# Kernel optimization log

Hardware: AMD Instinct MI355X
Metric: run time of the kernel (lower is better)

Reference implementation:

```python
import jax, jax.numpy as jnp
import numpy as np

N_E = 1024
E_DIM = 64
BETA = 0.25


def setup_inputs() -> dict:
    key = jax.random.key(0)
    k1, k2 = jax.random.split(key)
    z = jax.random.normal(k1, (32, 32, 32, E_DIM), dtype=jnp.float32)
    # torch init: uniform(-1/n_e, 1/n_e)
    codebook = jax.random.uniform(k2, (N_E, E_DIM), dtype=jnp.float32,
                                  minval=-1.0 / N_E, maxval=1.0 / N_E)
    return {"z": z, "codebook": codebook}


def reference(z, codebook):
    z_flat = z.reshape(-1, E_DIM)  # [N, e_dim]
    # squared euclidean distances: ||z||^2 + ||e||^2 - 2 z e^T
    d = (jnp.sum(z_flat ** 2, axis=1, keepdims=True)
         + jnp.sum(codebook ** 2, axis=1)
         - 2.0 * jnp.matmul(z_flat, codebook.T))  # [N, n_e]
    idx = jnp.argmin(d, axis=1)  # [N]
    z_q = codebook[idx].reshape(z.shape)
    sg = jax.lax.stop_gradient
    loss = jnp.mean((sg(z_q) - z) ** 2) + BETA * jnp.mean((z_q - sg(z)) ** 2)
    z_q_st = z + sg(z_q - z)  # straight-through estimator
    return z_q_st, idx, loss
```

## Files before the change

kernel.cpp:

```cpp
#include <hip/hip_runtime.h>

#define NROWS 32768
#define NE    1024
#define ED    64
#define CHUNK 256
#define NCH   (NE / CHUNK)
#define RPW   8

typedef float4 f4;

__global__ void vq_prep(const float* __restrict__ cb, float* __restrict__ ssq)
{
    int j = blockIdx.x * blockDim.x + threadIdx.x;
    const f4* crow = (const f4*)(cb + (size_t)j * ED);
    float v[ED];
#pragma unroll
    for (int i = 0; i < 16; ++i) {
        f4 t = crow[i];
        v[4*i+0] = t.x; v[4*i+1] = t.y; v[4*i+2] = t.z; v[4*i+3] = t.w;
    }
    {
#pragma clang fp contract(off)
        float r0 = v[0]*v[0], r1 = v[1]*v[1], r2 = v[2]*v[2], r3 = v[3]*v[3];
        float r4 = v[4]*v[4], r5 = v[5]*v[5], r6 = v[6]*v[6], r7 = v[7]*v[7];
#pragma unroll
        for (int i = 8; i < ED; i += 8) {
            r0 += v[i+0]*v[i+0]; r1 += v[i+1]*v[i+1];
            r2 += v[i+2]*v[i+2]; r3 += v[i+3]*v[i+3];
            r4 += v[i+4]*v[i+4]; r5 += v[i+5]*v[i+5];
            r6 += v[i+6]*v[i+6]; r7 += v[i+7]*v[i+7];
        }
        ssq[j] = ((r0+r1)+(r2+r3)) + ((r4+r5)+(r6+r7));
    }
}

__global__ __launch_bounds__(256, 2)
void vq_main(const float* __restrict__ z, const float* __restrict__ cb,
             const float* __restrict__ ssq, float* __restrict__ out,
             float* __restrict__ partials)
{
    __shared__ __align__(16) float et[ED * CHUNK];
    __shared__ __align__(16) float sqsh[NE];
    __shared__ int   idxsh[32];
    __shared__ float wsum[4];

    const int tid  = threadIdx.x;
    const int lane = tid & 63;
    const int w    = tid >> 6;
    const int w_u  = __builtin_amdgcn_readfirstlane(w);
    const int rowbase = blockIdx.x * 32;

    ((f4*)sqsh)[tid] = ((const f4*)ssq)[tid];

    float cn[RPW];
    {
        const int rl = lane >> 3;
        const int jj = lane & 7;
        const float* zr = z + (size_t)(rowbase + w_u * RPW + rl) * ED;
        float a;
        {
#pragma clang fp contract(off)
            a = 0.f;
#pragma unroll
            for (int i = 0; i < 8; ++i) { float v = zr[8*i + jj]; a += v*v; }
        }
        a += __shfl_xor(a, 1);
        a += __shfl_xor(a, 2);
        a += __shfl_xor(a, 4);
#pragma unroll
        for (int r = 0; r < RPW; ++r) cn[r] = __shfl(a, r * 8);
    }

    float bestv[RPW];
    int   besti[RPW];
#pragma unroll
    for (int r = 0; r < RPW; ++r) { bestv[r] = INFINITY; besti[r] = 0; }

    const f4* et4 = (const f4*)et;
    const float* zw = z + (size_t)(rowbase + w_u * RPW) * ED;

    for (int ch = 0; ch < NCH; ++ch) {
        __syncthreads();
        {
            const f4* crow = (const f4*)(cb + (size_t)(ch * CHUNK + tid) * ED);
#pragma unroll
            for (int i = 0; i < 16; ++i) {
                f4 t = crow[i];
                et[(4*i+0) * CHUNK + tid] = t.x;
                et[(4*i+1) * CHUNK + tid] = t.y;
                et[(4*i+2) * CHUNK + tid] = t.z;
                et[(4*i+3) * CHUNK + tid] = t.w;
            }
        }
        __syncthreads();

        f4 sv = ((const f4*)sqsh)[ch * 64 + lane];
        float svq[4] = {sv.x, sv.y, sv.z, sv.w};

        float acc[RPW][4];
#pragma unroll
        for (int r = 0; r < RPW; ++r)
            acc[r][0] = acc[r][1] = acc[r][2] = acc[r][3] = 0.f;

#pragma unroll 2
        for (int k4 = 0; k4 < 16; ++k4) {
            f4 e0 = et4[(4*k4+0) * 64 + lane];
            f4 e1 = et4[(4*k4+1) * 64 + lane];
            f4 e2 = et4[(4*k4+2) * 64 + lane];
            f4 e3 = et4[(4*k4+3) * 64 + lane];
            f4 z0 = *(const f4*)(zw + 0*ED + 4*k4);
            f4 z1 = *(const f4*)(zw + 1*ED + 4*k4);
            f4 z2 = *(const f4*)(zw + 2*ED + 4*k4);
            f4 z3 = *(const f4*)(zw + 3*ED + 4*k4);
            f4 z4 = *(const f4*)(zw + 4*ED + 4*k4);
            f4 z5 = *(const f4*)(zw + 5*ED + 4*k4);
            f4 z6 = *(const f4*)(zw + 6*ED + 4*k4);
            f4 z7 = *(const f4*)(zw + 7*ED + 4*k4);
#define ROWFMA(r, zz)                                                    \
            acc[r][0] = fmaf(zz.x, e0.x, acc[r][0]);                     \
            acc[r][1] = fmaf(zz.x, e0.y, acc[r][1]);                     \
            acc[r][2] = fmaf(zz.x, e0.z, acc[r][2]);                     \
            acc[r][3] = fmaf(zz.x, e0.w, acc[r][3]);                     \
            acc[r][0] = fmaf(zz.y, e1.x, acc[r][0]);                     \
            acc[r][1] = fmaf(zz.y, e1.y, acc[r][1]);                     \
            acc[r][2] = fmaf(zz.y, e1.z, acc[r][2]);                     \
            acc[r][3] = fmaf(zz.y, e1.w, acc[r][3]);                     \
            acc[r][0] = fmaf(zz.z, e2.x, acc[r][0]);                     \
            acc[r][1] = fmaf(zz.z, e2.y, acc[r][1]);                     \
            acc[r][2] = fmaf(zz.z, e2.z, acc[r][2]);                     \
            acc[r][3] = fmaf(zz.z, e2.w, acc[r][3]);                     \
            acc[r][0] = fmaf(zz.w, e3.x, acc[r][0]);                     \
            acc[r][1] = fmaf(zz.w, e3.y, acc[r][1]);                     \
            acc[r][2] = fmaf(zz.w, e3.z, acc[r][2]);                     \
            acc[r][3] = fmaf(zz.w, e3.w, acc[r][3]);
            ROWFMA(0, z0) ROWFMA(1, z1) ROWFMA(2, z2) ROWFMA(3, z3)
            ROWFMA(4, z4) ROWFMA(5, z5) ROWFMA(6, z6) ROWFMA(7, z7)
#undef ROWFMA
        }

        {
#pragma clang fp contract(off)
#pragma unroll
            for (int r = 0; r < RPW; ++r) {
#pragma unroll
                for (int q = 0; q < 4; ++q) {
                    float t1 = cn[r] + svq[q];
                    float d  = t1 - 2.0f * acc[r][q];
                    int j = ch * CHUNK + lane * 4 + q;
                    if (d < bestv[r]) { bestv[r] = d; besti[r] = j; }
                }
            }
        }
    }

    float lp = 0.f;
#pragma unroll
    for (int r = 0; r < RPW; ++r) {
        float v = bestv[r];
        int   i = besti[r];
#pragma unroll
        for (int m = 1; m < 64; m <<= 1) {
            float ov = __shfl_xor(v, m);
            int   oi = __shfl_xor(i, m);
            if (ov < v || (ov == v && oi < i)) { v = ov; i = oi; }
        }
        i &= (NE - 1);
        const int grow = rowbase + w * RPW + r;
        float zq, zz, diff, st;
        {
#pragma clang fp contract(off)
            zq   = cb[(size_t)i * ED + lane];
            zz   = z [(size_t)grow * ED + lane];
            diff = zq - zz;
            st   = zz + diff;
            lp  += diff * diff;
        }
        out[(size_t)grow * ED + lane] = st;
        if (lane == 0) idxsh[w * RPW + r] = i;
    }

#pragma unroll
    for (int m = 1; m < 64; m <<= 1) lp += __shfl_xor(lp, m);
    if (lane == 0) wsum[w] = lp;
    __syncthreads();

    if (tid < 32) {
        int iv = idxsh[tid] & (NE - 1);
        out[(size_t)NROWS * ED + rowbase + tid] = (float)iv;
    }
    if (tid == 0)
        partials[blockIdx.x] = (wsum[0] + wsum[1]) + (wsum[2] + wsum[3]);
}

__global__ void vq_finalize(const float* __restrict__ partials,
                            float* __restrict__ out)
{
    __shared__ float red[256];
    int t = threadIdx.x;
    float s = (partials[t] + partials[t + 256]) + (partials[t + 512] + partials[t + 768]);
    red[t] = s;
    __syncthreads();
    for (int m = 128; m > 0; m >>= 1) {
        if (t < m) red[t] += red[t + m];
        __syncthreads();
    }
    if (t == 0) {
        float mean = red[0] / (float)((size_t)NROWS * ED);
        out[(size_t)NROWS * ED + NROWS] = mean + 0.25f * mean;
    }
}

extern "C" void kernel_launch(void* const* d_in, const int* in_sizes, int n_in,
                              void* d_out, int out_size, void* d_ws, size_t ws_size,
                              hipStream_t stream)
{
    (void)in_sizes; (void)n_in; (void)out_size; (void)ws_size;
    const float* z  = (const float*)d_in[0];
    const float* cb = (const float*)d_in[1];
    float* out = (float*)d_out;
    float* ssq      = (float*)d_ws;
    float* partials = ssq + NE;

    vq_prep<<<4, 256, 0, stream>>>(cb, ssq);
    vq_main<<<1024, 256, 0, stream>>>(z, cb, ssq, out, partials);
    vq_finalize<<<1, 256, 0, stream>>>(partials, out);
}
```

Before: 87.80 us.

## Halve codebook chunk and per-lane columns to raise occupancy

Shrinks the shared-memory codebook chunk from 256 to 128 entries, so each lane computes 2 codes per row instead of 4, and raises launch bounds to 4 blocks per CU. The chunk load is split across two half-threads per code row. This cuts LDS use and accumulator registers so more waves fit per CU. In exchange there are twice as many chunk iterations and barriers, z reads are repeated per chunk, and each z value feeds fewer FMAs, lowering arithmetic intensity.

Result: faster. 74.38 us (-15.3%).

```diff
diff --git a/kernel.cpp b/kernel.cpp
--- a/kernel.cpp
+++ b/kernel.cpp
@@ -3,11 +3,12 @@
 #define NROWS 32768
 #define NE    1024
 #define ED    64
-#define CHUNK 256
+#define CHUNK 128
 #define NCH   (NE / CHUNK)
 #define RPW   8
 
 typedef float4 f4;
+typedef float2 f2;
 
 __global__ void vq_prep(const float* __restrict__ cb, float* __restrict__ ssq)
 {
@@ -34,7 +35,7 @@
     }
 }
 
-__global__ __launch_bounds__(256, 2)
+__global__ __launch_bounds__(256, 4)
 void vq_main(const float* __restrict__ z, const float* __restrict__ cb,
              const float* __restrict__ ssq, float* __restrict__ out,
              float* __restrict__ partials)
@@ -76,38 +77,41 @@
 #pragma unroll
     for (int r = 0; r < RPW; ++r) { bestv[r] = INFINITY; besti[r] = 0; }
 
-    const f4* et4 = (const f4*)et;
+    const f2* et2 = (const f2*)et;
     const float* zw = z + (size_t)(rowbase + w_u * RPW) * ED;
 
     for (int ch = 0; ch < NCH; ++ch) {
         __syncthreads();
         {
-            const f4* crow = (const f4*)(cb + (size_t)(ch * CHUNK + tid) * ED);
-#pragma unroll
-            for (int i = 0; i < 16; ++i) {
+            const int c = tid & 127;
+            const int h = tid >> 7;
+            const f4* crow = (const f4*)(cb + (size_t)(ch * CHUNK + c) * ED
+                                         + h * 32);
+#pragma unroll
+            for (int i = 0; i < 8; ++i) {
                 f4 t = crow[i];
-                et[(4*i+0) * CHUNK + tid] = t.x;
-                et[(4*i+1) * CHUNK + tid] = t.y;
-                et[(4*i+2) * CHUNK + tid] = t.z;
-                et[(4*i+3) * CHUNK + tid] = t.w;
+                const int dim = h * 32 + 4 * i;
+                et[(dim+0) * CHUNK + c] = t.x;
+                et[(dim+1) * CHUNK + c] = t.y;
+                et[(dim+2) * CHUNK + c] = t.z;
+                et[(dim+3) * CHUNK + c] = t.w;
             }
         }
         __syncthreads();
 
-        f4 sv = ((const f4*)sqsh)[ch * 64 + lane];
-        float svq[4] = {sv.x, sv.y, sv.z, sv.w};
-
-        float acc[RPW][4];
-#pragma unroll
-        for (int r = 0; r < RPW; ++r)
-            acc[r][0] = acc[r][1] = acc[r][2] = acc[r][3] = 0.f;
+        f2 sv = ((const f2*)sqsh)[ch * 64 + lane];
+        float svq[2] = {sv.x, sv.y};
+
+        float acc[RPW][2];
+#pragma unroll
+        for (int r = 0; r < RPW; ++r) acc[r][0] = acc[r][1] = 0.f;
 
 #pragma unroll 2
         for (int k4 = 0; k4 < 16; ++k4) {
-            f4 e0 = et4[(4*k4+0) * 64 + lane];
-            f4 e1 = et4[(4*k4+1) * 64 + lane];
-            f4 e2 = et4[(4*k4+2) * 64 + lane];
-            f4 e3 = et4[(4*k4+3) * 64 + lane];
+            f2 e0 = et2[(4*k4+0) * 64 + lane];
+            f2 e1 = et2[(4*k4+1) * 64 + lane];
+            f2 e2 = et2[(4*k4+2) * 64 + lane];
+            f2 e3 = et2[(4*k4+3) * 64 + lane];
             f4 z0 = *(const f4*)(zw + 0*ED + 4*k4);
             f4 z1 = *(const f4*)(zw + 1*ED + 4*k4);
             f4 z2 = *(const f4*)(zw + 2*ED + 4*k4);
@@ -119,20 +123,12 @@
 #define ROWFMA(r, zz)                                                    \
             acc[r][0] = fmaf(zz.x, e0.x, acc[r][0]);                     \
             acc[r][1] = fmaf(zz.x, e0.y, acc[r][1]);                     \
-            acc[r][2] = fmaf(zz.x, e0.z, acc[r][2]);                     \
-            acc[r][3] = fmaf(zz.x, e0.w, acc[r][3]);                     \
             acc[r][0] = fmaf(zz.y, e1.x, acc[r][0]);                     \
             acc[r][1] = fmaf(zz.y, e1.y, acc[r][1]);                     \
-            acc[r][2] = fmaf(zz.y, e1.z, acc[r][2]);                     \
-            acc[r][3] = fmaf(zz.y, e1.w, acc[r][3]);                     \
             acc[r][0] = fmaf(zz.z, e2.x, acc[r][0]);                     \
             acc[r][1] = fmaf(zz.z, e2.y, acc[r][1]);                     \
-            acc[r][2] = fmaf(zz.z, e2.z, acc[r][2]);                     \
-            acc[r][3] = fmaf(zz.z, e2.w, acc[r][3]);                     \
             acc[r][0] = fmaf(zz.w, e3.x, acc[r][0]);                     \
-            acc[r][1] = fmaf(zz.w, e3.y, acc[r][1]);                     \
-            acc[r][2] = fmaf(zz.w, e3.z, acc[r][2]);                     \
-            acc[r][3] = fmaf(zz.w, e3.w, acc[r][3]);
+            acc[r][1] = fmaf(zz.w, e3.y, acc[r][1]);
             ROWFMA(0, z0) ROWFMA(1, z1) ROWFMA(2, z2) ROWFMA(3, z3)
             ROWFMA(4, z4) ROWFMA(5, z5) ROWFMA(6, z6) ROWFMA(7, z7)
 #undef ROWFMA
@@ -143,10 +139,10 @@
 #pragma unroll
             for (int r = 0; r < RPW; ++r) {
 #pragma unroll
-                for (int q = 0; q < 4; ++q) {
+                for (int q = 0; q < 2; ++q) {
                     float t1 = cn[r] + svq[q];
                     float d  = t1 - 2.0f * acc[r][q];
-                    int j = ch * CHUNK + lane * 4 + q;
+                    int j = ch * CHUNK + lane * 2 + q;
                     if (d < bestv[r]) { bestv[r] = d; besti[r] = j; }
                 }
             }
```
